# Kernel optimization log

Hardware: AMD Instinct MI355X
Metric: run time of the kernel (lower is better)

Reference implementation:

```python
import jax, jax.numpy as jnp
import numpy as np

N = 200      # nodes (fixed by Linear(200,100) on x.T)
E = 8000     # edges
NFEAT, NHID, NCLASS = 8192, 2048, 512


def _cheb_conv(x, edge_index, edge_weight, W, b):
    """PyG ChebConv (K=3, sym norm, lambda_max=2): L_hat = -D^{-1/2} A D^{-1/2}.
    T0 = x, T1 = L_hat x, T2 = 2 L_hat T1 - T0; out = sum_k T_k @ W[k] + b."""
    row, col = edge_index[0], edge_index[1]
    deg = jax.ops.segment_sum(edge_weight, row, num_segments=N)
    safe = jnp.where(deg > 0, deg, 1.0)
    dinv = jnp.where(deg > 0, 1.0 / jnp.sqrt(safe), 0.0)
    norm = -dinv[row] * edge_weight * dinv[col]  # [E]

    def lap(z):  # messages from source j=row to target i=col
        return jax.ops.segment_sum(norm[:, None] * z[row], col, num_segments=N)

    T1 = lap(x)
    T2 = 2.0 * lap(T1) - x
    return x @ W[0] + T1 @ W[1] + T2 @ W[2] + b


def _forward_single(x, ei, ew, W1, b1, W2, b2):
    h = jax.nn.relu(_cheb_conv(x, ei, ew, W1, b1))
    # dropout is identity in eval mode
    return _cheb_conv(h, ei, ew, W2, b2)  # [N, NCLASS]


def _classifier(z, Wc1, bc1, Wc2, bc2, Wc3, bc3):
    h = jax.nn.relu(z @ Wc1.T + bc1)
    h = jax.nn.relu(h @ Wc2.T + bc2)
    return h @ Wc3.T + bc3  # [NCLASS, 1]


def setup_inputs() -> dict:
    key = jax.random.key(0)
    ks = jax.random.split(key, 12)
    inp = {
        'x1': jax.random.normal(ks[0], (N, NFEAT), jnp.float32),
        'edge_index1': jax.random.randint(ks[1], (2, E), 0, N, jnp.int64),
        'edge_attr1': jax.random.uniform(ks[2], (E,), jnp.float32),
        'x2': jax.random.normal(ks[3], (N, NFEAT), jnp.float32),
        'edge_index2': jax.random.randint(ks[4], (2, E), 0, N, jnp.int64),
        'edge_attr2': jax.random.uniform(ks[5], (E,), jnp.float32),
        'W1': jax.random.normal(ks[6], (3, NFEAT, NHID), jnp.float32) * (NFEAT ** -0.5),
        'b1': jnp.zeros((NHID,), jnp.float32),
        'W2': jax.random.normal(ks[7], (3, NHID, NCLASS), jnp.float32) * (NHID ** -0.5),
        'b2': jnp.zeros((NCLASS,), jnp.float32),
        'Wc1': jax.random.normal(ks[8], (100, 200), jnp.float32) * (200 ** -0.5),
        'bc1': jnp.zeros((100,), jnp.float32),
        'Wc2': jax.random.normal(ks[9], (50, 100), jnp.float32) * (100 ** -0.5),
        'bc2': jnp.zeros((50,), jnp.float32),
        'Wc3': jax.random.normal(ks[10], (1, 50), jnp.float32) * (50 ** -0.5),
        'bc3': jnp.zeros((1,), jnp.float32),
    }
    return inp


def reference(x1, edge_index1, edge_attr1, x2, edge_index2, edge_attr2,
              W1, b1, W2, b2, Wc1, bc1, Wc2, bc2, Wc3, bc3):
    o1 = _forward_single(x1, edge_index1, edge_attr1, W1, b1, W2, b2)
    o2 = _forward_single(x2, edge_index2, edge_attr2, W1, b1, W2, b2)
    out1 = _classifier(o1.T, Wc1, bc1, Wc2, bc2, Wc3, bc3)  # [NCLASS, 1]
    out2 = _classifier(o2.T, Wc1, bc1, Wc2, bc2, Wc3, bc3)
    return out1, out2
```

## Files before the change

kernel.cpp:

```cpp
#include <hip/hip_runtime.h>

typedef __attribute__((ext_vector_type(8))) short short8;
typedef __attribute__((ext_vector_type(4))) float f32x4;
typedef __attribute__((ext_vector_type(2))) float f32x2;
typedef __attribute__((ext_vector_type(4))) unsigned int u32x4;

#define NNODES 200
#define NEDGE  8000
#define NF1    8192
#define NH     2048
#define NCL    512
#define K1     24576
#define K2     6144
#define MR     448
#define MV     400
#define PV     400
#define KC1    16
#define BK1    1536
#define KC2    16
#define BK2    384
#define M1T    224

#define OFF_P1  0ull
#define SZ_P1   ((unsigned long long)KC1*PV*NH*4)
#define OFF_P2  (OFF_P1 + SZ_P1)
#define SZ_P2   ((unsigned long long)KC2*PV*NCL*4)
#define OFF_A1  (OFF_P2 + SZ_P2)
#define SZ_A1   ((unsigned long long)MR*K1*2)
#define OFF_A2  (OFF_A1 + SZ_A1)
#define SZ_A2   ((unsigned long long)MR*K2*2)
#define OFF_LD  (OFF_A2 + SZ_A2)
#define OFF_LL  (OFF_LD + 320000ull)
#define OFF_Z   OFF_P1

static __device__ __forceinline__ unsigned short f2bf(float f) {
  unsigned int u = __float_as_uint(f);
  unsigned int r = (u + 0x7fffu + ((u >> 16) & 1u)) >> 16;
  return (unsigned short)r;
}
static __device__ __forceinline__ unsigned packbf(float a, float b) {
  return (unsigned)f2bf(a) | ((unsigned)f2bf(b) << 16);
}

__global__ void k_zero(f32x4* p1, int n1, f32x4* p2, int n2, f32x4* p3, int n3) {
  int i = blockIdx.x * 256 + threadIdx.x;
  f32x4 z = {0.f, 0.f, 0.f, 0.f};
  if (i < n1) p1[i] = z;
  i -= n1;
  if (i >= 0 && i < n2) p2[i] = z;
  i -= n2;
  if (i >= 0 && i < n3) p3[i] = z;
}

__global__ __launch_bounds__(1024)
void k_graph(const int* __restrict__ ei1, const float* __restrict__ ew1,
             const int* __restrict__ ei2, const float* __restrict__ ew2,
             float* __restrict__ Ld) {
  __shared__ float degs[NNODES];
  const int g = blockIdx.x;
  const int* ei = g ? ei2 : ei1;
  const float* ew = g ? ew2 : ew1;
  const int t = threadIdx.x;

  if (t < NNODES) degs[t] = 0.f;
  __syncthreads();
  for (int e = t; e < NEDGE; e += 1024) atomicAdd(&degs[ei[e]], ew[e]);
  __syncthreads();
  if (t < NNODES) {
    float d = degs[t];
    degs[t] = d > 0.f ? 1.0f / sqrtf(d) : 0.f;
  }
  __syncthreads();
  float* Lg = Ld + (size_t)g * NNODES * NNODES;
  for (int e = t; e < NEDGE; e += 1024) {
    int r = ei[e], c = ei[NEDGE + e];
    float nrm = -degs[r] * ew[e] * degs[c];
    atomicAdd(Lg + (size_t)c * NNODES + r, nrm);
  }
}

__global__ void k_LL(const float* __restrict__ Ld, unsigned short* __restrict__ LLb) {
  int b = blockIdx.x;
  int g = b / NNODES, i = b % NNODES;
  __shared__ float Lr[NNODES];
  const float* Lg = Ld + (size_t)g * NNODES * NNODES;
  int t = threadIdx.x;
  if (t < NNODES) Lr[t] = Lg[i * NNODES + t];
  __syncthreads();
  if (t < NNODES) {
    float acc = 0.f;
    for (int k = 0; k < NNODES; ++k) acc = fmaf(Lr[k], Lg[k * NNODES + t], acc);
    unsigned short* LLg = LLb + (size_t)g * MR * 224;
    LLg[(size_t)i * 224 + t] = f2bf(Lr[t]);
    LLg[(size_t)(NNODES + i) * 224 + t] = f2bf(2.f * acc - (i == t ? 1.f : 0.f));
  }
}

__global__ void k_t0(const float* __restrict__ x1, const float* __restrict__ x2,
                     unsigned short* __restrict__ A1) {
  int gid = blockIdx.x * 256 + threadIdx.x;
  int row = gid / (NF1 / 8);
  int c8 = (gid % (NF1 / 8)) * 8;
  const float* xp = (row < NNODES ? x1 + (size_t)row * NF1
                                  : x2 + (size_t)(row - NNODES) * NF1) + c8;
  f32x4 a = *(const f32x4*)xp;
  f32x4 b = *(const f32x4*)(xp + 4);
  u32x4 o;
  o[0] = packbf(a[0], a[1]);
  o[1] = packbf(a[2], a[3]);
  o[2] = packbf(b[0], b[1]);
  o[3] = packbf(b[2], b[3]);
  *(u32x4*)(A1 + (size_t)row * K1 + c8) = o;
}

__global__ __launch_bounds__(256, 1)
void k_abuild(const unsigned short* __restrict__ LLb, const unsigned short* __restrict__ Asrc,
              unsigned short* __restrict__ Adst, const int Nf, const int Ka) {
  __shared__ __align__(16) unsigned short XF[7][4][64][8];
  const int g = blockIdx.x & 1;
  const int nt = blockIdx.x >> 1;
  const int nbase = nt * 64;
  const int t = threadIdx.x;

  #pragma unroll
  for (int it = 0; it < 14; ++it) {
    const int pos = it * 256 + t;
    const int j = pos >> 4;
    const int n4 = (pos & 15) * 4;
    unsigned long long v = 0ull;
    if (j < NNODES)
      v = *(const unsigned long long*)(Asrc + (size_t)(g * NNODES + j) * Ka + nbase + n4);
    const int ks = j >> 5, kg = (j >> 3) & 3, jj = j & 7;
    #pragma unroll
    for (int e = 0; e < 4; ++e) {
      const int nn = n4 + e;
      XF[ks][nn >> 4][(nn & 15) + 16 * kg][jj] = (unsigned short)(v >> (16 * e));
    }
  }
  __syncthreads();

  const int w = t >> 6, lane = t & 63;
  const int lm = lane & 15, lk8 = (lane >> 4) * 8;
  f32x4 acc[7][4];
  #pragma unroll
  for (int i = 0; i < 7; ++i)
    #pragma unroll
    for (int j = 0; j < 4; ++j) acc[i][j] = (f32x4){0.f, 0.f, 0.f, 0.f};

  const unsigned short* LLg = LLb + (size_t)g * MR * 224;
  #pragma unroll
  for (int ks = 0; ks < 7; ++ks) {
    short8 bfr[4];
    #pragma unroll
    for (int nf = 0; nf < 4; ++nf) bfr[nf] = *(const short8*)&XF[ks][nf][lane][0];
    short8 af[7];
    #pragma unroll
    for (int mf = 0; mf < 7; ++mf)
      af[mf] = *(const short8*)(LLg + (size_t)(w * 112 + mf * 16 + lm) * 224 + ks * 32 + lk8);
    #pragma unroll
    for (int mf = 0; mf < 7; ++mf)
      #pragma unroll
      for (int nf = 0; nf < 4; ++nf)
        acc[mf][nf] = __builtin_amdgcn_mfma_f32_16x16x32_bf16(af[mf], bfr[nf], acc[mf][nf], 0, 0, 0);
  }

  const int lr4 = (lane >> 4) * 4;
  #pragma unroll
  for (int mf = 0; mf < 7; ++mf) {
    #pragma unroll
    for (int ri = 0; ri < 4; ++ri) {
      const int m = w * 112 + mf * 16 + lr4 + ri;
      if (m < MV) {
        const int drow = g * NNODES + (m < NNODES ? m : m - NNODES);
        const size_t dbase = (size_t)drow * Ka + (m < NNODES ? Nf : 2 * Nf) + nbase + lm;
        #pragma unroll
        for (int nf = 0; nf < 4; ++nf)
          Adst[dbase + nf * 16] = f2bf(acc[mf][nf][ri]);
      }
    }
  }
}

__global__ __launch_bounds__(256, 2)
void k_gemm1(const float* __restrict__ W, const unsigned short* __restrict__ A,
             float* __restrict__ P) {
  constexpr int Nn = NH;
  constexpr int BK = BK1;
  constexpr int NF = 4;
  constexpr int NFW = 2;
  constexpr int ABUF = M1T * 128;
  constexpr int BSTRIDE = NF * 1024;
  constexpr int WBUF = 2 * BSTRIDE;
  __shared__ __align__(16) unsigned short Atile[2 * M1T * 64];
  __shared__ __align__(16) unsigned short Wt[2 * NF * 1024];

  const int t = threadIdx.x;
  const int w = t >> 6, lane = t & 63;
  const int wm = w >> 1, wn = w & 1;
  const int lm = lane & 15, l4 = lane >> 4;
  const int b = blockIdx.x;
  const int kc = b & 15;
  const int m  = (b >> 4) & 1;
  const int nt = b >> 5;
  const int kbase = kc * BK;
  const int nbase = nt * 64;
  const int nks = BK >> 6;

  const int gb = ((t * 16) & 127) ^ (((t >> 3) & 7) << 4);
  const char* Ab = (const char*)A + ((size_t)(m * M1T + (t >> 3)) * K1 + kbase) * 2 + gb;
  const size_t CSTEP = (size_t)32 * K1 * 2;

  const int kk0 = (t >> 4) * 4;
  const int colb = (t & 15) * 4;
  const float* Wg = W + (size_t)(kbase + kk0) * Nn + nbase + colb;
  int offWl[2][4];
  #pragma unroll
  for (int p = 0; p < 2; ++p) {
    const int kk = kk0 + 2 * p;
    const int ks0 = kk >> 5, kg0 = (kk >> 3) & 3, jj1 = (kk & 7) >> 1;
    #pragma unroll
    for (int e = 0; e < 4; ++e) {
      const int nn = colb + e;
      const int nf = nn >> 4;
      const int ln = ((nn & 15) + 16 * kg0) ^ (nf & 3);
      offWl[p][e] = ((ks0 * NF + nf) * 64 + ln) * 4 + jj1;
    }
  }

  const int aBase = (wm * 112 + lm) * 128 + ((l4 * 16) ^ ((lm & 7) << 4));
  int bAddr[NFW];
  #pragma unroll
  for (int nf = 0; nf < NFW; ++nf) {
    const int nfg = wn * NFW + nf;
    bAddr[nf] = nfg * 1024 + (lane ^ (nfg & 3)) * 16;
  }

  f32x4 acc[7][NFW];
  #pragma unroll
  for (int i = 0; i < 7; ++i)
    #pragma unroll
    for (int j = 0; j < NFW; ++j) acc[i][j] = (f32x4){0.f, 0.f, 0.f, 0.f};

  u32x4 areg[7];
  f32x4 wv[4];

  auto loadW = [&](int kt) {
    const float* p = Wg + (size_t)kt * 64 * Nn;
    #pragma unroll
    for (int r = 0; r < 4; ++r)
      wv[r] = __builtin_nontemporal_load((const f32x4*)(p + (size_t)r * Nn));
  };
  auto loadA = [&](int kt) {
    #pragma unroll
    for (int c = 0; c < 7; ++c)
      areg[c] = *(const u32x4*)(Ab + c * CSTEP + (size_t)kt * 128);
  };
  auto storeA = [&](int buf) {
    #pragma unroll
    for (int c = 0; c < 7; ++c)
      *(u32x4*)((char*)Atile + buf * ABUF + c * 4096 + t * 16) = areg[c];
  };
  auto storeW = [&](int buf) {
    unsigned* w32 = (unsigned*)Wt + buf * (WBUF / 4);
    #pragma unroll
    for (int p = 0; p < 2; ++p)
      #pragma unroll
      for (int e = 0; e < 4; ++e)
        w32[offWl[p][e]] = packbf(wv[2 * p][e], wv[2 * p + 1][e]);
  };
  auto compute = [&](int buf, int ks) {
    short8 bfr[NFW];
    #pragma unroll
    for (int nf = 0; nf < NFW; ++nf)
      bfr[nf] = *(const short8*)((const char*)Wt + buf * WBUF + bAddr[nf] + ks * BSTRIDE);
    short8 af[7];
    #pragma unroll
    for (int mf = 0; mf < 7; ++mf)
      af[mf] = *(const short8*)((const char*)Atile + buf * ABUF + ((aBase + mf * 2048) ^ (ks * 64)));
    #pragma unroll
    for (int mf = 0; mf < 7; ++mf)
      #pragma unroll
      for (int nf = 0; nf < NFW; ++nf)
        acc[mf][nf] = __builtin_amdgcn_mfma_f32_16x16x32_bf16(af[mf], bfr[nf], acc[mf][nf], 0, 0, 0);
  };

  loadW(0);
  loadA(0);
  storeA(0);
  storeW(0);
  __syncthreads();

  for (int kt = 0; kt < nks; ++kt) {
    const int buf = kt & 1;
    const bool more = (kt + 1 < nks);
    if (more) loadW(kt + 1);
    compute(buf, 0);
    if (more) loadA(kt + 1);
    compute(buf, 1);
    if (more) {
      storeA(buf ^ 1);
      storeW(buf ^ 1);
    }
    __syncthreads();
  }

  float* Pk = P + ((size_t)kc * PV) * Nn + nbase;
  #pragma unroll
  for (int mf = 0; mf < 7; ++mf) {
    const int row0 = m * M1T + wm * 112 + mf * 16 + l4 * 4;
    #pragma unroll
    for (int ri = 0; ri < 4; ++ri) {
      const int row = row0 + ri;
      if (row < MV) {
        #pragma unroll
        for (int nf = 0; nf < NFW; ++nf) {
          const int col = (wn * NFW + nf) * 16 + lm;
          __builtin_nontemporal_store(acc[mf][nf][ri], Pk + (size_t)row * Nn + col);
        }
      }
    }
  }
}

template <int BN, int KA, int KC>
__global__ __launch_bounds__(512, 2)
void k_gemm(const float* __restrict__ W, const unsigned short* __restrict__ A,
            float* __restrict__ P, const int Nn, const int BK) {
  constexpr int NF = BN / 16;
  constexpr int NFW = BN / 32;
  constexpr int CW = BN / 16;
  constexpr int ABUF = MR * 128;
  constexpr int BSTRIDE = NF * 1024;
  constexpr int WBUF = 2 * BSTRIDE;
  __shared__ __align__(16) unsigned short Atile[2 * MR * 64];
  __shared__ __align__(16) unsigned short Wt[2 * NF * 1024];

  const int t = threadIdx.x;
  const int w = t >> 6, lane = t & 63;
  const int wm = w >> 1, wn = w & 1;
  const int lm = lane & 15;
  const int l4 = lane >> 4;
  const int kc = blockIdx.x % KC;
  const int nt = blockIdx.x / KC;
  const int kbase = kc * BK;
  const int nbase = nt * BN;
  const int nks = BK >> 6;

  const int arow0 = t >> 3;
  const int agb = ((t * 16) & 127) ^ ((arow0 & 7) << 4);
  const char* Ab = (const char*)A + (size_t)kbase * 2 + (size_t)arow0 * (KA * 2) + agb;
  const size_t CSTEP = (size_t)64 * KA * 2;

  const int kk0 = (t >> 4) * 2;
  const int colb = (t & 15) * CW;
  const float* Wg = W + (size_t)(kbase + kk0) * Nn + nbase + colb;
  int offWl[CW];
  {
    const int ks0 = kk0 >> 5, kg0 = (kk0 >> 3) & 3, jj1 = (kk0 & 7) >> 1;
    #pragma unroll
    for (int e = 0; e < CW; ++e) {
      const int nn = colb + e;
      const int nf = nn >> 4;
      const int ln = ((nn & 15) + 16 * kg0) ^ (nf & 3);
      offWl[e] = ((ks0 * NF + nf) * 64 + ln) * 4 + jj1;
    }
  }

  const int aBase = (wm * 112 + lm) * 128 + ((l4 * 16) ^ ((lm & 7) << 4));
  int bAddr[NFW];
  #pragma unroll
  for (int nf = 0; nf < NFW; ++nf) {
    const int nfg = wn * NFW + nf;
    bAddr[nf] = nfg * 1024 + (lane ^ (nfg & 3)) * 16;
  }

  f32x4 acc[7][NFW];
  #pragma unroll
  for (int i = 0; i < 7; ++i)
    #pragma unroll
    for (int j = 0; j < NFW; ++j) acc[i][j] = (f32x4){0.f, 0.f, 0.f, 0.f};

  u32x4 areg[7];
  f32x2 w0s, w1s;

  auto loadW = [&](int kt) {
    const float* p = Wg + (size_t)kt * 64 * Nn;
    w0s = __builtin_nontemporal_load((const f32x2*)p);
    w1s = __builtin_nontemporal_load((const f32x2*)(p + Nn));
  };
  auto loadA = [&](int kt) {
    #pragma unroll
    for (int c = 0; c < 7; ++c)
      areg[c] = *(const u32x4*)(Ab + c * CSTEP + (size_t)kt * 128);
  };
  auto storeA = [&](int buf) {
    #pragma unroll
    for (int c = 0; c < 7; ++c)
      *(u32x4*)((char*)Atile + buf * ABUF + c * 8192 + t * 16) = areg[c];
  };
  auto storeW = [&](int buf) {
    unsigned* w32 = (unsigned*)Wt + buf * (WBUF / 4);
    #pragma unroll
    for (int e = 0; e < CW; ++e)
      w32[offWl[e]] = packbf(w0s[e & 1], w1s[e & 1]);
  };

  loadW(0);
  loadA(0);
  storeA(0);
  storeW(0);
  __syncthreads();

  for (int kt = 0; kt < nks; ++kt) {
    const int buf = kt & 1;
    const bool more = (kt + 1 < nks);
    if (more) loadW(kt + 1);

    #pragma unroll
    for (int ks = 0; ks < 2; ++ks) {
      short8 bfr[NFW];
      #pragma unroll
      for (int nf = 0; nf < NFW; ++nf)
        bfr[nf] = *(const short8*)((const char*)Wt + buf * WBUF + bAddr[nf] + ks * BSTRIDE);
      const int abx = (aBase ^ (ks * 64)) + buf * ABUF;
      short8 af[7];
      #pragma unroll
      for (int mf = 0; mf < 7; ++mf)
        af[mf] = *(const short8*)((const char*)Atile + abx + mf * 2048);
      #pragma unroll
      for (int mf = 0; mf < 7; ++mf)
        #pragma unroll
        for (int nf = 0; nf < NFW; ++nf)
          acc[mf][nf] = __builtin_amdgcn_mfma_f32_16x16x32_bf16(af[mf], bfr[nf], acc[mf][nf], 0, 0, 0);
      if (ks == 0 && more) loadA(kt + 1);
    }

    if (more) {
      storeA(buf ^ 1);
      storeW(buf ^ 1);
    }
    __syncthreads();
  }

  float* Pk = P + ((size_t)kc * PV) * Nn + nbase;
  #pragma unroll
  for (int mf = 0; mf < 7; ++mf) {
    const int row0 = wm * 112 + mf * 16 + l4 * 4;
    #pragma unroll
    for (int ri = 0; ri < 4; ++ri) {
      const int row = row0 + ri;
      if (row < MV) {
        #pragma unroll
        for (int nf = 0; nf < NFW; ++nf) {
          const int col = (wn * NFW + nf) * 16 + lm;
          __builtin_nontemporal_store(acc[mf][nf][ri], Pk + (size_t)row * Nn + col);
        }
      }
    }
  }
}

__global__ void k_ep1(const float* __restrict__ P1, const float* __restrict__ b1,
                      unsigned short* __restrict__ A2) {
  int gid = blockIdx.x * 256 + threadIdx.x;
  int row = gid / (NH / 4);
  int c = (gid % (NH / 4)) * 4;
  f32x4 s = {0.f, 0.f, 0.f, 0.f};
  #pragma unroll
  for (int kc = 0; kc < KC1; ++kc)
    s += __builtin_nontemporal_load((const f32x4*)(P1 + ((size_t)kc * PV + row) * NH + c));
  const f32x4 b = *(const f32x4*)(b1 + c);
  unsigned long long pack = 0;
  #pragma unroll
  for (int i = 0; i < 4; ++i) {
    float v = s[i] + b[i];
    pack |= (unsigned long long)f2bf(v > 0.f ? v : 0.f) << (16 * i);
  }
  *(unsigned long long*)(A2 + (size_t)row * K2 + c) = pack;
}

__global__ __launch_bounds__(256)
void k_zsum(const float* __restrict__ P2, const float* __restrict__ b2,
            float* __restrict__ zt) {
  __shared__ float tile[8][264];
  const int b = blockIdx.x;
  const int g = b / 50;
  const int r2 = b % 50;
  const int j0 = (r2 >> 1) * 8;
  const int ch = (r2 & 1) * 256;
  const int t = threadIdx.x;
  const int j = t >> 5;
  const int c0 = (t & 31) * 8;
  const int row = g * NNODES + j0 + j;

  #pragma unroll
  for (int ci = 0; ci < 2; ++ci) {
    const int c = c0 + ci * 4;
    f32x4 s = *(const f32x4*)(b2 + ch + c);
    #pragma unroll
    for (int kc = 0; kc < KC2; ++kc)
      s += __builtin_nontemporal_load((const f32x4*)(P2 + ((size_t)kc * PV + row) * NCL + ch + c));
    *(f32x4*)&tile[j][c] = s;
  }
  __syncthreads();

  f32x4 lo, hi;
  #pragma unroll
  for (int e = 0; e < 4; ++e) { lo[e] = tile[e][t]; hi[e] = tile[4 + e][t]; }
  float* zr = zt + ((size_t)g * NCL + ch + t) * 200 + j0;
  *(f32x4*)zr = lo;
  *(f32x4*)(zr + 4) = hi;
}

__global__ __launch_bounds__(256)
void k_cls2(const float* __restrict__ zt,
            const float* __restrict__ Wc1, const float* __restrict__ bc1,
            const float* __restrict__ Wc2, const float* __restrict__ bc2,
            const float* __restrict__ Wc3, const float* __restrict__ bc3,
            float* __restrict__ outp) {
  __shared__ float W1s[100 * 201];
  __shared__ float W2s[50 * 101];
  __shared__ float zs[4][200];
  __shared__ float h1s[4][104];
  __shared__ float h2s[4][56];
  const int g = blockIdx.x >> 7;
  const int t = threadIdx.x;
  const int w = t >> 6, lane = t & 63;
  const int r = (blockIdx.x & 127) * 4 + w;

  for (int i = t; i < 20000; i += 256) {
    const int c = i / 200, j = i - c * 200;
    W1s[c * 201 + j] = Wc1[i];
  }
  for (int i = t; i < 5000; i += 256) {
    const int c = i / 100, j = i - c * 100;
    W2s[c * 101 + j] = Wc2[i];
  }
  const float* zr = zt + ((size_t)g * NCL + r) * 200;
  #pragma unroll
  for (int i = 0; i < 4; ++i) {
    const int idx = i * 64 + lane;
    if (idx < 200) zs[w][idx] = zr[idx];
  }
  __syncthreads();

  {
    const int c1 = lane + 64;
    const int c1m = (c1 < 100) ? c1 : 99;
    float a0 = bc1[lane];
    float a1 = bc1[c1m];
    #pragma unroll 4
    for (int j = 0; j < 200; ++j) {
      const float zv = zs[w][j];
      a0 = fmaf(zv, W1s[lane * 201 + j], a0);
      a1 = fmaf(zv, W1s[c1m * 201 + j], a1);
    }
    h1s[w][lane] = a0 > 0.f ? a0 : 0.f;
    if (c1 < 100) h1s[w][c1] = a1 > 0.f ? a1 : 0.f;
  }
  __syncthreads();

  {
    const int c2 = (lane < 50) ? lane : 49;
    float b = bc2[c2];
    #pragma unroll 4
    for (int c = 0; c < 100; ++c) b = fmaf(h1s[w][c], W2s[c2 * 101 + c], b);
    if (lane < 50) h2s[w][lane] = b > 0.f ? b : 0.f;
  }
  __syncthreads();

  {
    float v = (lane < 50) ? h2s[w][lane] * Wc3[lane] : 0.f;
    #pragma unroll
    for (int off = 32; off >= 1; off >>= 1) v += __shfl_down(v, off);
    if (lane == 0) outp[g * NCL + r] = v + bc3[0];
  }
}

extern "C" void kernel_launch(void* const* d_in, const int* in_sizes, int n_in,
                              void* d_out, int out_size, void* d_ws, size_t ws_size,
                              hipStream_t stream) {
  const float* x1  = (const float*)d_in[0];
  const int*   ei1 = (const int*)d_in[1];
  const float* ea1 = (const float*)d_in[2];
  const float* x2  = (const float*)d_in[3];
  const int*   ei2 = (const int*)d_in[4];
  const float* ea2 = (const float*)d_in[5];
  const float* W1  = (const float*)d_in[6];
  const float* b1  = (const float*)d_in[7];
  const float* W2  = (const float*)d_in[8];
  const float* b2  = (const float*)d_in[9];
  const float* Wc1 = (const float*)d_in[10];
  const float* bc1 = (const float*)d_in[11];
  const float* Wc2 = (const float*)d_in[12];
  const float* bc2 = (const float*)d_in[13];
  const float* Wc3 = (const float*)d_in[14];
  const float* bc3 = (const float*)d_in[15];
  float* outp = (float*)d_out;

  char* ws = (char*)d_ws;
  float*          P1  = (float*)(ws + OFF_P1);
  float*          P2  = (float*)(ws + OFF_P2);
  unsigned short* A1  = (unsigned short*)(ws + OFF_A1);
  unsigned short* A2  = (unsigned short*)(ws + OFF_A2);
  float*          Ld  = (float*)(ws + OFF_LD);
  unsigned short* LLb = (unsigned short*)(ws + OFF_LL);
  float*          zt  = (float*)(ws + OFF_Z);

  k_zero<<<897, 256, 0, stream>>>(
      (f32x4*)(ws + OFF_LD), 45088,
      (f32x4*)(ws + OFF_A1 + (size_t)MV * K1 * 2), 147456,
      (f32x4*)(ws + OFF_A2 + (size_t)MV * K2 * 2), 36864);

  k_graph<<<2, 1024, 0, stream>>>(ei1, ea1, ei2, ea2, Ld);
  k_LL<<<400, 256, 0, stream>>>(Ld, LLb);
  k_t0<<<1600, 256, 0, stream>>>(x1, x2, A1);
  k_abuild<<<(NF1 / 64) * 2, 256, 0, stream>>>(LLb, A1, A1, NF1, K1);
  k_gemm1<<<1024, 256, 0, stream>>>(W1, A1, P1);
  k_ep1<<<800, 256, 0, stream>>>(P1, b1, A2);
  k_abuild<<<(NH / 64) * 2, 256, 0, stream>>>(LLb, A2, A2, NH, K2);
  k_gemm<32, K2, KC2><<<KC2 * (NCL / 32), 512, 0, stream>>>(W2, A2, P2, NCL, BK2);
  k_zsum<<<100, 256, 0, stream>>>(P2, b2, zt);
  k_cls2<<<256, 256, 0, stream>>>(zt, Wc1, bc1, Wc2, bc2, Wc3, bc3, outp);
}
```

Measured before the change: 212.8 us.

## Retile layer-1 GEMM to full-M 512-thread blocks with deeper W prefetch

The first big GEMM now uses 512-thread blocks that cover all 448 rows and a 128-wide N tile, instead of splitting M in two. This removes the duplicated W1 streaming across the two M halves. W loads are prefetched two k-steps ahead with a ping-pong register set, and the barrier is a lighter LDS-only wait. Separately, the two-block graph normalization kernel is split into parallel degree and Laplacian-build kernels with global atomics. The trade-off is higher register and LDS pressure and fewer blocks in the GEMM grid.

```diff
diff --git a/kernel.cpp b/kernel.cpp
--- a/kernel.cpp
+++ b/kernel.cpp
@@ -19,7 +19,6 @@
 #define BK1    1536
 #define KC2    16
 #define BK2    384
-#define M1T    224
 
 #define OFF_P1  0ull
 #define SZ_P1   ((unsigned long long)KC1*PV*NH*4)
@@ -29,7 +28,8 @@
 #define SZ_A1   ((unsigned long long)MR*K1*2)
 #define OFF_A2  (OFF_A1 + SZ_A1)
 #define SZ_A2   ((unsigned long long)MR*K2*2)
-#define OFF_LD  (OFF_A2 + SZ_A2)
+#define OFF_DEG (OFF_A2 + SZ_A2)
+#define OFF_LD  (OFF_DEG + 2048)
 #define OFF_LL  (OFF_LD + 320000ull)
 #define OFF_Z   OFF_P1
 
@@ -40,6 +40,13 @@
 }
 static __device__ __forceinline__ unsigned packbf(float a, float b) {
   return (unsigned)f2bf(a) | ((unsigned)f2bf(b) << 16);
+}
+
+static __device__ __forceinline__ void bar_lds() {
+  asm volatile("s_waitcnt lgkmcnt(0)" ::: "memory");
+  __builtin_amdgcn_sched_barrier(0);
+  __builtin_amdgcn_s_barrier();
+  __builtin_amdgcn_sched_barrier(0);
 }
 
 __global__ void k_zero(f32x4* p1, int n1, f32x4* p2, int n2, f32x4* p3, int n3) {
@@ -52,31 +59,31 @@
   if (i >= 0 && i < n3) p3[i] = z;
 }
 
-__global__ __launch_bounds__(1024)
-void k_graph(const int* __restrict__ ei1, const float* __restrict__ ew1,
-             const int* __restrict__ ei2, const float* __restrict__ ew2,
-             float* __restrict__ Ld) {
-  __shared__ float degs[NNODES];
-  const int g = blockIdx.x;
+__global__ void k_deg(const int* __restrict__ ei1, const float* __restrict__ ew1,
+                      const int* __restrict__ ei2, const float* __restrict__ ew2,
+                      float* __restrict__ deg) {
+  int e = blockIdx.x * 256 + threadIdx.x;
+  if (e >= 2 * NEDGE) return;
+  int g = e / NEDGE, k = e % NEDGE;
   const int* ei = g ? ei2 : ei1;
   const float* ew = g ? ew2 : ew1;
-  const int t = threadIdx.x;
-
-  if (t < NNODES) degs[t] = 0.f;
-  __syncthreads();
-  for (int e = t; e < NEDGE; e += 1024) atomicAdd(&degs[ei[e]], ew[e]);
-  __syncthreads();
-  if (t < NNODES) {
-    float d = degs[t];
-    degs[t] = d > 0.f ? 1.0f / sqrtf(d) : 0.f;
-  }
-  __syncthreads();
-  float* Lg = Ld + (size_t)g * NNODES * NNODES;
-  for (int e = t; e < NEDGE; e += 1024) {
-    int r = ei[e], c = ei[NEDGE + e];
-    float nrm = -degs[r] * ew[e] * degs[c];
-    atomicAdd(Lg + (size_t)c * NNODES + r, nrm);
-  }
+  atomicAdd(deg + g * NNODES + ei[k], ew[k]);
+}
+
+__global__ void k_buildL(const int* __restrict__ ei1, const float* __restrict__ ew1,
+                         const int* __restrict__ ei2, const float* __restrict__ ew2,
+                         const float* __restrict__ deg, float* __restrict__ Ld) {
+  int e = blockIdx.x * 256 + threadIdx.x;
+  if (e >= 2 * NEDGE) return;
+  int g = e / NEDGE, k = e % NEDGE;
+  const int* ei = g ? ei2 : ei1;
+  const float* ew = g ? ew2 : ew1;
+  int r = ei[k], c = ei[NEDGE + k];
+  float dr = deg[g * NNODES + r], dc = deg[g * NNODES + c];
+  float ir = dr > 0.f ? 1.0f / sqrtf(dr) : 0.f;
+  float ic = dc > 0.f ? 1.0f / sqrtf(dc) : 0.f;
+  float nrm = -ir * ew[k] * ic;
+  atomicAdd(Ld + ((size_t)g * NNODES + c) * NNODES + r, nrm);
 }
 
 __global__ void k_LL(const float* __restrict__ Ld, unsigned short* __restrict__ LLb) {
@@ -181,49 +188,47 @@
   }
 }
 
-__global__ __launch_bounds__(256, 2)
+struct WS { f32x4 a, b, c, d; };
+
+__global__ __launch_bounds__(512, 2)
 void k_gemm1(const float* __restrict__ W, const unsigned short* __restrict__ A,
              float* __restrict__ P) {
-  constexpr int Nn = NH;
-  constexpr int BK = BK1;
-  constexpr int NF = 4;
-  constexpr int NFW = 2;
-  constexpr int ABUF = M1T * 128;
+  constexpr int Nn = NH, BK = BK1, KA = K1, KC = KC1;
+  constexpr int NF = 8, NFW = 4, CW = 8;
+  constexpr int ABUF = MR * 128;
   constexpr int BSTRIDE = NF * 1024;
   constexpr int WBUF = 2 * BSTRIDE;
-  __shared__ __align__(16) unsigned short Atile[2 * M1T * 64];
+  __shared__ __align__(16) unsigned short Atile[2 * MR * 64];
   __shared__ __align__(16) unsigned short Wt[2 * NF * 1024];
 
   const int t = threadIdx.x;
   const int w = t >> 6, lane = t & 63;
   const int wm = w >> 1, wn = w & 1;
-  const int lm = lane & 15, l4 = lane >> 4;
-  const int b = blockIdx.x;
-  const int kc = b & 15;
-  const int m  = (b >> 4) & 1;
-  const int nt = b >> 5;
+  const int lm = lane & 15;
+  const int l4 = lane >> 4;
+  const int kc = blockIdx.x % KC;
+  const int nt = blockIdx.x / KC;
   const int kbase = kc * BK;
-  const int nbase = nt * 64;
-  const int nks = BK >> 6;
-
-  const int gb = ((t * 16) & 127) ^ (((t >> 3) & 7) << 4);
-  const char* Ab = (const char*)A + ((size_t)(m * M1T + (t >> 3)) * K1 + kbase) * 2 + gb;
-  const size_t CSTEP = (size_t)32 * K1 * 2;
-
-  const int kk0 = (t >> 4) * 4;
-  const int colb = (t & 15) * 4;
+  const int nbase = nt * 128;
+  constexpr int nks = BK >> 6;
+
+  const int arow0 = t >> 3;
+  const int agb = ((t * 16) & 127) ^ ((arow0 & 7) << 4);
+  const char* Ab = (const char*)A + (size_t)kbase * 2 + (size_t)arow0 * (KA * 2) + agb;
+  const size_t CSTEP = (size_t)64 * KA * 2;
+
+  const int kk0 = (t >> 4) * 2;
+  const int colb = (t & 15) * CW;
   const float* Wg = W + (size_t)(kbase + kk0) * Nn + nbase + colb;
-  int offWl[2][4];
-  #pragma unroll
-  for (int p = 0; p < 2; ++p) {
-    const int kk = kk0 + 2 * p;
-    const int ks0 = kk >> 5, kg0 = (kk >> 3) & 3, jj1 = (kk & 7) >> 1;
-    #pragma unroll
-    for (int e = 0; e < 4; ++e) {
+  int offWl[CW];
+  {
+    const int ks0 = kk0 >> 5, kg0 = (kk0 >> 3) & 3, jj1 = (kk0 & 7) >> 1;
+    #pragma unroll
+    for (int e = 0; e < CW; ++e) {
       const int nn = colb + e;
       const int nf = nn >> 4;
       const int ln = ((nn & 15) + 16 * kg0) ^ (nf & 3);
-      offWl[p][e] = ((ks0 * NF + nf) * 64 + ln) * 4 + jj1;
+      offWl[e] = ((ks0 * NF + nf) * 64 + ln) * 4 + jj1;
     }
   }
 
@@ -242,72 +247,82 @@
     for (int j = 0; j < NFW; ++j) acc[i][j] = (f32x4){0.f, 0.f, 0.f, 0.f};
 
   u32x4 areg[7];
-  f32x4 wv[4];
-
-  auto loadW = [&](int kt) {
-    const float* p = Wg + (size_t)kt * 64 * Nn;
-    #pragma unroll
-    for (int r = 0; r < 4; ++r)
-      wv[r] = __builtin_nontemporal_load((const f32x4*)(p + (size_t)r * Nn));
-  };
+  WS sA, sB;
+
   auto loadA = [&](int kt) {
     #pragma unroll
     for (int c = 0; c < 7; ++c)
       areg[c] = *(const u32x4*)(Ab + c * CSTEP + (size_t)kt * 128);
   };
+  auto loadWs = [&](int kt, WS& s) {
+    const float* p = Wg + (size_t)kt * 64 * Nn;
+    s.a = __builtin_nontemporal_load((const f32x4*)p);
+    s.b = __builtin_nontemporal_load((const f32x4*)(p + 4));
+    s.c = __builtin_nontemporal_load((const f32x4*)(p + Nn));
+    s.d = __builtin_nontemporal_load((const f32x4*)(p + Nn + 4));
+  };
   auto storeA = [&](int buf) {
     #pragma unroll
     for (int c = 0; c < 7; ++c)
-      *(u32x4*)((char*)Atile + buf * ABUF + c * 4096 + t * 16) = areg[c];
-  };
-  auto storeW = [&](int buf) {
+      *(u32x4*)((char*)Atile + buf * ABUF + c * 8192 + t * 16) = areg[c];
+  };
+  auto storeWs = [&](const WS& s, int buf) {
     unsigned* w32 = (unsigned*)Wt + buf * (WBUF / 4);
     #pragma unroll
-    for (int p = 0; p < 2; ++p)
-      #pragma unroll
-      for (int e = 0; e < 4; ++e)
-        w32[offWl[p][e]] = packbf(wv[2 * p][e], wv[2 * p + 1][e]);
-  };
-  auto compute = [&](int buf, int ks) {
-    short8 bfr[NFW];
-    #pragma unroll
-    for (int nf = 0; nf < NFW; ++nf)
-      bfr[nf] = *(const short8*)((const char*)Wt + buf * WBUF + bAddr[nf] + ks * BSTRIDE);
-    short8 af[7];
-    #pragma unroll
-    for (int mf = 0; mf < 7; ++mf)
-      af[mf] = *(const short8*)((const char*)Atile + buf * ABUF + ((aBase + mf * 2048) ^ (ks * 64)));
-    #pragma unroll
-    for (int mf = 0; mf < 7; ++mf)
+    for (int e = 0; e < CW; ++e) {
+      float lo = (e < 4) ? s.a[e & 3] : s.b[e & 3];
+      float hi = (e < 4) ? s.c[e & 3] : s.d[e & 3];
+      w32[offWl[e]] = packbf(lo, hi);
+    }
+  };
+  auto compute = [&](int buf) {
+    #pragma unroll
+    for (int ks = 0; ks < 2; ++ks) {
+      short8 bfr[NFW];
       #pragma unroll
       for (int nf = 0; nf < NFW; ++nf)
-        acc[mf][nf] = __builtin_amdgcn_mfma_f32_16x16x32_bf16(af[mf], bfr[nf], acc[mf][nf], 0, 0, 0);
-  };
-
-  loadW(0);
-  loadA(0);
-  storeA(0);
-  storeW(0);
-  __syncthreads();
-
-  for (int kt = 0; kt < nks; ++kt) {
+        bfr[nf] = *(const short8*)((const char*)Wt + buf * WBUF + bAddr[nf] + ks * BSTRIDE);
+      const int abx = (aBase ^ (ks * 64)) + buf * ABUF;
+      short8 af[7];
+      #pragma unroll
+      for (int mf = 0; mf < 7; ++mf)
+        af[mf] = *(const short8*)((const char*)Atile + abx + mf * 2048);
+      #pragma unroll
+      for (int mf = 0; mf < 7; ++mf)
+        #pragma unroll
+        for (int nf = 0; nf < NFW; ++nf)
+          acc[mf][nf] = __builtin_amdgcn_mfma_f32_16x16x32_bf16(af[mf], bfr[nf], acc[mf][nf], 0, 0, 0);
+    }
+  };
+  auto body = [&](int kt, WS& cur, WS& oth) {
+    const bool more = kt + 1 < nks;
     const int buf = kt & 1;
-    const bool more = (kt + 1 < nks);
-    if (more) loadW(kt + 1);
-    compute(buf, 0);
     if (more) loadA(kt + 1);
-    compute(buf, 1);
+    if (kt + 2 < nks) loadWs(kt + 2, oth);
+    compute(buf);
     if (more) {
       storeA(buf ^ 1);
-      storeW(buf ^ 1);
-    }
-    __syncthreads();
+      storeWs(cur, buf ^ 1);
+      bar_lds();
+    }
+  };
+
+  loadA(0);
+  loadWs(0, sA);
+  storeA(0);
+  storeWs(sA, 0);
+  loadWs(1, sA);
+  bar_lds();
+
+  for (int kt = 0; kt < nks; kt += 2) {
+    body(kt, sA, sB);
+    body(kt + 1, sB, sA);
   }
 
   float* Pk = P + ((size_t)kc * PV) * Nn + nbase;
   #pragma unroll
   for (int mf = 0; mf < 7; ++mf) {
-    const int row0 = m * M1T + wm * 112 + mf * 16 + l4 * 4;
+    const int row0 = wm * 112 + mf * 16 + l4 * 4;
     #pragma unroll
     for (int ri = 0; ri < 4; ++ri) {
       const int row = row0 + ri;
@@ -603,20 +618,22 @@
   float*          P2  = (float*)(ws + OFF_P2);
   unsigned short* A1  = (unsigned short*)(ws + OFF_A1);
   unsigned short* A2  = (unsigned short*)(ws + OFF_A2);
+  float*          deg = (float*)(ws + OFF_DEG);
   float*          Ld  = (float*)(ws + OFF_LD);
   unsigned short* LLb = (unsigned short*)(ws + OFF_LL);
   float*          zt  = (float*)(ws + OFF_Z);
 
   k_zero<<<897, 256, 0, stream>>>(
-      (f32x4*)(ws + OFF_LD), 45088,
+      (f32x4*)(ws + OFF_DEG), 45216,
       (f32x4*)(ws + OFF_A1 + (size_t)MV * K1 * 2), 147456,
       (f32x4*)(ws + OFF_A2 + (size_t)MV * K2 * 2), 36864);
 
-  k_graph<<<2, 1024, 0, stream>>>(ei1, ea1, ei2, ea2, Ld);
+  k_deg<<<63, 256, 0, stream>>>(ei1, ea1, ei2, ea2, deg);
+  k_buildL<<<63, 256, 0, stream>>>(ei1, ea1, ei2, ea2, deg, Ld);
   k_LL<<<400, 256, 0, stream>>>(Ld, LLb);
   k_t0<<<1600, 256, 0, stream>>>(x1, x2, A1);
   k_abuild<<<(NF1 / 64) * 2, 256, 0, stream>>>(LLb, A1, A1, NF1, K1);
-  k_gemm1<<<1024, 256, 0, stream>>>(W1, A1, P1);
+  k_gemm1<<<KC1 * (NH / 128), 512, 0, stream>>>(W1, A1, P1);
   k_ep1<<<800, 256, 0, stream>>>(P1, b1, A2);
   k_abuild<<<(NH / 64) * 2, 256, 0, stream>>>(LLb, A2, A2, NH, K2);
   k_gemm<32, K2, KC2><<<KC2 * (NCL / 32), 512, 0, stream>>>(W2, A2, P2, NCL, BK2);
```

Result: faster. 192.7 us (-9.5%).
